# Performance work log

Measured on AMD Instinct MI355X. Metric: run time of the kernel, lower is better.

Reference implementation:

```python
import jax, jax.numpy as jnp
import numpy as np

ALPHA = 8.3  # depth-similarity decay from Depth-aware CNN
K = 3        # kernel size
PAD = 1      # padding (stride=1, dilation=1)


def _patches(x, k, pad):
    """Extract kxk stride-1 patches. x: (B,C,H,W) -> (B,C,k,k,H,W)."""
    B, C, H, W = x.shape
    xp = jnp.pad(x, ((0, 0), (0, 0), (pad, pad), (pad, pad)))
    rows = []
    for i in range(k):
        cols = [xp[:, :, i:i + H, j:j + W] for j in range(k)]
        rows.append(jnp.stack(cols, axis=2))          # (B,C,k,H,W)
    return jnp.stack(rows, axis=2)                     # (B,C,k,k,H,W)


def setup_inputs() -> dict:
    key = jax.random.key(0)
    k1, k2, k3 = jax.random.split(key, 3)
    B, Cin, H, W = 8, 512, 64, 64
    Cout = 64
    x = jax.random.normal(k1, (B, Cin, H, W), dtype=jnp.float32)
    depth = jax.random.uniform(k2, (B, 1, H, W), dtype=jnp.float32)
    stdv = 1.0 / np.sqrt(Cin * K * K)
    weight = jax.random.uniform(k3, (Cout, Cin, K, K), dtype=jnp.float32,
                                minval=-stdv, maxval=stdv)
    return {"input": x, "depth": depth, "weight": weight}


def reference(input, depth, weight):
    # depth-modulated conv: out(p0) = sum_pn w(pn) * x(p0+pn) * exp(-a*|d(p0)-d(p0+pn)|)
    xpat = _patches(input, K, PAD)                 # (B,Cin,K,K,H,W)
    dpat = _patches(depth, K, PAD)                 # (B,1,K,K,H,W)
    d0 = depth[:, :, None, None, :, :]             # center depth (B,1,1,1,H,W)
    gate = jnp.exp(-ALPHA * jnp.abs(d0 - dpat))    # (B,1,K,K,H,W)
    out = jnp.einsum('ocij,bcijhw->bohw', weight, xpat * gate)
    return out
```

## Files before the change

kernel.cpp:

```cpp
#include <hip/hip_runtime.h>
#include <math.h>

#define ALPHA 8.3f
#define XSZ   16896
#define WSZ   36864
#define BUFSZ 53760

typedef short v8s  __attribute__((ext_vector_type(8)));
typedef float v16f __attribute__((ext_vector_type(16)));
typedef float v4f  __attribute__((ext_vector_type(4)));

static __device__ __forceinline__ unsigned short f2bf(float f) {
    unsigned int u = __float_as_uint(f);
    u = (u + 0x7fffu + ((u >> 16) & 1u)) >> 16;
    return (unsigned short)u;
}

static __device__ __forceinline__ void async16(const void* g, void* l) {
    __builtin_amdgcn_global_load_lds(
        (const __attribute__((address_space(1))) unsigned int*)g,
        (__attribute__((address_space(3))) unsigned int*)l, 16, 0, 0);
}

__global__ __launch_bounds__(256) void prep_weights(const float* __restrict__ w,
                                                    unsigned short* __restrict__ wt) {
    const int i = blockIdx.x * 256 + threadIdx.x;
    if (i >= 294912) return;
    const int j    = i & 7;
    const int lane = (i >> 3) & 63;
    const int F    = i >> 9;
    const int kc   = F & 1;
    const int mt   = (F >> 1) & 1;
    const int tq   = F >> 2;
    const int tap  = tq % 9;
    const int ss   = tq / 9;
    const int o    = mt * 32 + (lane & 31);
    const int cin  = ss * 32 + kc * 16 + (lane >> 5) * 8 + j;
    wt[i] = f2bf(w[(o * 512 + cin) * 9 + tap]);
}

__global__ __launch_bounds__(384)
void depthconv_v15(const float* __restrict__ x,
                   const float* __restrict__ depth,
                   const unsigned short* __restrict__ wt,
                   float* __restrict__ out) {
    __shared__ __align__(16) char smem[2 * BUFSZ];

    const int bx   = blockIdx.x;
    const int xcd  = bx & 7;
    const int i0   = bx >> 3;
    const int b    = i0 & 7;
    const int h0   = (xcd * 4 + (i0 >> 3)) * 2;

    const int tid  = threadIdx.x;
    const int wid  = tid >> 6;
    const int lane = tid & 63;
    const int l31  = lane & 31;
    const int half = lane >> 5;
    const int rt   = wid & 1;
    const int di   = wid >> 1;

    const float* xb = x + (size_t)b * 2097152;
    const float* xsrc[3];
    int  goff[3];
    bool gval[3], gact[3];
#pragma unroll
    for (int it = 0; it < 3; ++it) {
        const int g_i = it * 384 + tid;
        const bool act = (g_i < 1056);
        const int p_ = g_i / 264;
        const int s_ = g_i - p_ * 264;
        const int r_ = s_ / 66, c_ = s_ - r_ * 66;
        const int hh = h0 - 1 + r_, ww = c_ - 1;
        const bool val = act && hh >= 0 && hh < 64 && ww >= 0 && ww < 64;
        gact[it] = act;
        gval[it] = val;
        goff[it] = g_i * 16;
        xsrc[it] = val ? (xb + (size_t)(p_ * 8) * 4096 + hh * 64 + ww) : xb;
    }

#define XLOAD(SS, V)                                                             \
    {                                                                            \
        const size_t adv = (size_t)(SS) * 131072;       \
        _Pragma("unroll")                                                        \
        for (int it = 0; it < 3; ++it)                                           \
            _Pragma("unroll")                                                    \
            for (int e = 0; e < 8; ++e)                                          \
                V[it][e] = gval[it] ? xsrc[it][adv + (size_t)e * 4096] : 0.f;    \
    }
#define XWRITE(V, BSEL)                                                          \
    {                                                                            \
        char* dx = smem + (BSEL) * BUFSZ;                                        \
        _Pragma("unroll")                                                        \
        for (int it = 0; it < 3; ++it)                                           \
            if (gact[it]) {                                                      \
                uint4 u;                                                         \
                u.x = f2bf(V[it][0]) | ((unsigned)f2bf(V[it][1]) << 16);         \
                u.y = f2bf(V[it][2]) | ((unsigned)f2bf(V[it][3]) << 16);         \
                u.z = f2bf(V[it][4]) | ((unsigned)f2bf(V[it][5]) << 16);         \
                u.w = f2bf(V[it][6]) | ((unsigned)f2bf(V[it][7]) << 16);         \
                *(uint4*)(dx + goff[it]) = u;                                    \
            }                                                                    \
    }
#define WISSUE(SS, BSEL)                                                         \
    {                                                                            \
        char* dw = smem + (BSEL) * BUFSZ + XSZ;                                  \
        const char* ws = (const char*)wt + (size_t)(SS) * WSZ;                   \
        _Pragma("unroll")                                                        \
        for (int k = 0; k < 6; ++k)                                              \
            async16(ws + (size_t)(k * 384 + tid) * 16,                           \
                    dw + (k * 384 + tid) * 16);                                  \
    }

    float gt[2][3];
    {
        const float* dp = depth + (size_t)b * 4096;
        const int hq = h0 + rt;
        const int hn = hq + di - 1;
#pragma unroll
        for (int n = 0; n < 2; ++n) {
            const int wq = n * 32 + l31;
            const float d0 = dp[hq * 64 + wq];
#pragma unroll
            for (int dj = 0; dj < 3; ++dj) {
                const int wn = wq + dj - 1;
                const float dn = (hn >= 0 && hn < 64 && wn >= 0 && wn < 64)
                                     ? dp[hn * 64 + wn] : 0.f;
                gt[n][dj] = __expf(-ALPHA * fabsf(d0 - dn));
            }
        }
    }

    v16f a00[3], a01[3], a10[3], a11[3];
#pragma unroll
    for (int d = 0; d < 3; ++d)
#pragma unroll
        for (int r = 0; r < 16; ++r) { a00[d][r] = 0.f; a01[d][r] = 0.f;
                                       a10[d][r] = 0.f; a11[d][r] = 0.f; }

    const int aOff = XSZ + di * 12288 + lane * 16;
    const int bOff = (half * 264 + (rt + di) * 66 + l31) * 16;

    float v[3][8];
    WISSUE(0, 0);
    XLOAD(0, v);
    XWRITE(v, 0);

    for (int ss = 0; ss < 16; ++ss) {
        __syncthreads();
        const int cur = ss & 1;
        const int nxt = cur ^ 1;
        if (ss < 15) {
            WISSUE(ss + 1, nxt);
            XLOAD(ss + 1, v);
        }
        const char* ba = smem + cur * BUFSZ + aOff;
        const char* bb = smem + cur * BUFSZ + bOff;
#pragma unroll
        for (int dj = 0; dj < 3; ++dj) {
#pragma unroll
            for (int kc = 0; kc < 2; ++kc) {
                const v8s w0 = *(const v8s*)(ba + ((dj * 2 + 0) * 2 + kc) * 1024);
                const v8s w1 = *(const v8s*)(ba + ((dj * 2 + 1) * 2 + kc) * 1024);
                const v8s x0 = *(const v8s*)(bb + kc * 8448 + (0 * 32 + dj) * 16);
                const v8s x1 = *(const v8s*)(bb + kc * 8448 + (1 * 32 + dj) * 16);
                a00[dj] = __builtin_amdgcn_mfma_f32_32x32x16_bf16(w0, x0, a00[dj], 0, 0, 0);
                a01[dj] = __builtin_amdgcn_mfma_f32_32x32x16_bf16(w1, x0, a01[dj], 0, 0, 0);
                a10[dj] = __builtin_amdgcn_mfma_f32_32x32x16_bf16(w0, x1, a10[dj], 0, 0, 0);
                a11[dj] = __builtin_amdgcn_mfma_f32_32x32x16_bf16(w1, x1, a11[dj], 0, 0, 0);
            }
        }
        if (ss < 15) XWRITE(v, nxt);
    }

#pragma unroll
    for (int r = 0; r < 16; ++r) {
        a00[0][r] = gt[0][0] * a00[0][r];
        a00[0][r] = fmaf(gt[0][1], a00[1][r], a00[0][r]);
        a00[0][r] = fmaf(gt[0][2], a00[2][r], a00[0][r]);
        a01[0][r] = gt[0][0] * a01[0][r];
        a01[0][r] = fmaf(gt[0][1], a01[1][r], a01[0][r]);
        a01[0][r] = fmaf(gt[0][2], a01[2][r], a01[0][r]);
        a10[0][r] = gt[1][0] * a10[0][r];
        a10[0][r] = fmaf(gt[1][1], a10[1][r], a10[0][r]);
        a10[0][r] = fmaf(gt[1][2], a10[2][r], a10[0][r]);
        a11[0][r] = gt[1][0] * a11[0][r];
        a11[0][r] = fmaf(gt[1][1], a11[1][r], a11[0][r]);
        a11[0][r] = fmaf(gt[1][2], a11[2][r], a11[0][r]);
    }

    __syncthreads();
    float* red = (float*)smem;
    const int rbase = rt * 4096 + lane * 4;
#define EPI_STORE(ACC, N, MT)                                                    \
    _Pragma("unroll")                                                            \
    for (int qd = 0; qd < 4; ++qd) {                                             \
        v4f vv; vv[0] = ACC[0][qd * 4]; vv[1] = ACC[0][qd * 4 + 1];              \
        vv[2] = ACC[0][qd * 4 + 2]; vv[3] = ACC[0][qd * 4 + 3];                  \
        *(v4f*)&red[rbase + ((N) * 2 + (MT)) * 1024 + qd * 256] = vv;            \
    }
#define EPI_ADD(ACC, N, MT)                                                      \
    _Pragma("unroll")                                                            \
    for (int qd = 0; qd < 4; ++qd) {                                             \
        v4f vv = *(const v4f*)&red[rbase + ((N) * 2 + (MT)) * 1024 + qd * 256];  \
        vv[0] += ACC[0][qd * 4];     vv[1] += ACC[0][qd * 4 + 1];                \
        vv[2] += ACC[0][qd * 4 + 2]; vv[3] += ACC[0][qd * 4 + 3];                \
        *(v4f*)&red[rbase + ((N) * 2 + (MT)) * 1024 + qd * 256] = vv;            \
    }
    if (di == 2) {
        EPI_STORE(a00, 0, 0) EPI_STORE(a01, 0, 1) EPI_STORE(a10, 1, 0) EPI_STORE(a11, 1, 1)
    }
    __syncthreads();
    if (di == 1) {
        EPI_ADD(a00, 0, 0) EPI_ADD(a01, 0, 1) EPI_ADD(a10, 1, 0) EPI_ADD(a11, 1, 1)
    }
    __syncthreads();
    if (di == 0) {
        float* ob = out + (size_t)b * 262144 + (h0 + rt) * 64;
#define EPI_OUT(ACC, N, MT)                                                      \
    _Pragma("unroll")                                                            \
    for (int qd = 0; qd < 4; ++qd) {                                             \
        const v4f vv = *(const v4f*)&red[rbase + ((N) * 2 + (MT)) * 1024 + qd * 256]; \
        _Pragma("unroll")                                                        \
        for (int j = 0; j < 4; ++j) {                                            \
            const int rg = qd * 4 + j;                                           \
            const int o = (MT) * 32 + (rg & 3) + 8 * (rg >> 2) + 4 * half;       \
            ob[(size_t)o * 4096 + (N) * 32 + l31] = ACC[0][rg] + vv[j];          \
        }                                                                        \
    }
        EPI_OUT(a00, 0, 0) EPI_OUT(a01, 0, 1) EPI_OUT(a10, 1, 0) EPI_OUT(a11, 1, 1)
    }
}

extern "C" void kernel_launch(void* const* d_in, const int* in_sizes, int n_in,
                              void* d_out, int out_size, void* d_ws, size_t ws_size,
                              hipStream_t stream) {
    const float* x      = (const float*)d_in[0];
    const float* depth  = (const float*)d_in[1];
    const float* weight = (const float*)d_in[2];
    float* out = (float*)d_out;

    unsigned short* wtb = (unsigned short*)d_ws;

    prep_weights<<<1152, 256, 0, stream>>>(weight, wtb);
    depthconv_v15<<<256, 384, 0, stream>>>(x, depth, wtb, out);
}
```

Before: 133.0 us.

## Split output channels across twice the waves and software-pipeline loads with manual waitcnt

Doubles the block to 768 threads so each wave owns one 32-channel output tile instead of two, halving its accumulator registers. The staging loop becomes a two-register-set software pipeline: the next slice's global loads are issued before the current compute, and raw s_waitcnt plus s_barrier replace __syncthreads. Depth-gate computation moves after the main loop to shorten live ranges. This aims to hide memory latency and raise per-CU wave count, at the cost of fragile hand-counted vmcnt values and more LDS reads of the shared x tiles.

```diff
diff --git a/kernel.cpp b/kernel.cpp
--- a/kernel.cpp
+++ b/kernel.cpp
@@ -39,8 +39,8 @@
     wt[i] = f2bf(w[(o * 512 + cin) * 9 + tap]);
 }
 
-__global__ __launch_bounds__(384)
-void depthconv_v15(const float* __restrict__ x,
+__global__ __launch_bounds__(768, 3)
+void depthconv_v16(const float* __restrict__ x,
                    const float* __restrict__ depth,
                    const unsigned short* __restrict__ wt,
                    float* __restrict__ out) {
@@ -57,60 +57,132 @@
     const int lane = tid & 63;
     const int l31  = lane & 31;
     const int half = lane >> 5;
-    const int rt   = wid & 1;
-    const int di   = wid >> 1;
+    const int mt   = wid & 1;
+    const int rt   = (wid >> 1) & 1;
+    const int di   = wid >> 2;
 
     const float* xb = x + (size_t)b * 2097152;
-    const float* xsrc[3];
-    int  goff[3];
-    bool gval[3], gact[3];
-#pragma unroll
-    for (int it = 0; it < 3; ++it) {
-        const int g_i = it * 384 + tid;
-        const bool act = (g_i < 1056);
-        const int p_ = g_i / 264;
-        const int s_ = g_i - p_ * 264;
-        const int r_ = s_ / 66, c_ = s_ - r_ * 66;
-        const int hh = h0 - 1 + r_, ww = c_ - 1;
-        const bool val = act && hh >= 0 && hh < 64 && ww >= 0 && ww < 64;
-        gact[it] = act;
-        gval[it] = val;
-        goff[it] = g_i * 16;
-        xsrc[it] = val ? (xb + (size_t)(p_ * 8) * 4096 + hh * 64 + ww) : xb;
-    }
-
-#define XLOAD(SS, V)                                                             \
-    {                                                                            \
-        const size_t adv = (size_t)(SS) * 131072;       \
-        _Pragma("unroll")                                                        \
-        for (int it = 0; it < 3; ++it)                                           \
+
+    int goff0, goff1; bool val0, val1, act1;
+    const float* pX0; const float* pX1;
+    {
+        const int g0 = tid;
+        const int p0 = g0 / 264, s0 = g0 - p0 * 264;
+        const int r0 = s0 / 66,  c0 = s0 - r0 * 66;
+        const int hh0 = h0 - 1 + r0, ww0 = c0 - 1;
+        val0  = (hh0 >= 0 && hh0 < 64 && ww0 >= 0 && ww0 < 64);
+        goff0 = g0 * 16;
+        pX0   = val0 ? (xb + (size_t)(p0 * 8) * 4096 + hh0 * 64 + ww0) : xb;
+
+        act1 = (tid < 288);
+        const int g1 = act1 ? (768 + tid) : tid;
+        const int p1 = g1 / 264, s1 = g1 - p1 * 264;
+        const int r1 = s1 / 66,  c1 = s1 - r1 * 66;
+        const int hh1 = h0 - 1 + r1, ww1 = c1 - 1;
+        val1  = (hh1 >= 0 && hh1 < 64 && ww1 >= 0 && ww1 < 64);
+        goff1 = g1 * 16;
+        pX1   = val1 ? (xb + (size_t)(p1 * 8) * 4096 + hh1 * 64 + ww1) : xb;
+    }
+    const char* pW = (const char*)wt;
+
+#define XLOAD(V)                                                                 \
+    {                                                                            \
+        _Pragma("unroll")                                                        \
+        for (int e = 0; e < 8; ++e) V[e]     = pX0[(size_t)e * 4096];            \
+        _Pragma("unroll")                                                        \
+        for (int e = 0; e < 8; ++e) V[8 + e] = pX1[(size_t)e * 4096];            \
+        pX0 += 131072; pX1 += 131072;                                            \
+    }
+#define XWRITE(V, BSEL)                                                          \
+    {                                                                            \
+        char* dx = smem + (BSEL) * BUFSZ;                                        \
+        uint4 u0;                                                                \
+        u0.x = f2bf(V[0]) | ((unsigned)f2bf(V[1]) << 16);                        \
+        u0.y = f2bf(V[2]) | ((unsigned)f2bf(V[3]) << 16);                        \
+        u0.z = f2bf(V[4]) | ((unsigned)f2bf(V[5]) << 16);                        \
+        u0.w = f2bf(V[6]) | ((unsigned)f2bf(V[7]) << 16);                        \
+        if (!val0) { u0.x = 0u; u0.y = 0u; u0.z = 0u; u0.w = 0u; }               \
+        *(uint4*)(dx + goff0) = u0;                                              \
+        if (act1) {                                                              \
+            uint4 u1;                                                            \
+            u1.x = f2bf(V[8])  | ((unsigned)f2bf(V[9])  << 16);                  \
+            u1.y = f2bf(V[10]) | ((unsigned)f2bf(V[11]) << 16);                  \
+            u1.z = f2bf(V[12]) | ((unsigned)f2bf(V[13]) << 16);                  \
+            u1.w = f2bf(V[14]) | ((unsigned)f2bf(V[15]) << 16);                  \
+            if (!val1) { u1.x = 0u; u1.y = 0u; u1.z = 0u; u1.w = 0u; }           \
+            *(uint4*)(dx + goff1) = u1;                                          \
+        }                                                                        \
+    }
+#define WISSUE(BSEL)                                                             \
+    {                                                                            \
+        char* dw = smem + (BSEL) * BUFSZ + XSZ;                                  \
+        _Pragma("unroll")                                                        \
+        for (int k = 0; k < 3; ++k)                                              \
+            async16(pW + (size_t)(k * 768 + tid) * 16,                           \
+                    dw + (k * 768 + tid) * 16);                                  \
+        pW += WSZ;                                                               \
+    }
+
+    v16f A0[3], A1[3];
+#pragma unroll
+    for (int d = 0; d < 3; ++d)
+#pragma unroll
+        for (int r = 0; r < 16; ++r) { A0[d][r] = 0.f; A1[d][r] = 0.f; }
+
+    const int aOff = XSZ + di * 12288 + mt * 2048 + lane * 16;
+    const int bOff = (half * 264 + (rt + di) * 66 + l31) * 16;
+
+#define COMPUTE(BSEL)                                                            \
+    {                                                                            \
+        const char* ba = smem + (BSEL) * BUFSZ + aOff;                           \
+        const char* bb = smem + (BSEL) * BUFSZ + bOff;                           \
+        _Pragma("unroll")                                                        \
+        for (int dj = 0; dj < 3; ++dj)                                           \
             _Pragma("unroll")                                                    \
-            for (int e = 0; e < 8; ++e)                                          \
-                V[it][e] = gval[it] ? xsrc[it][adv + (size_t)e * 4096] : 0.f;    \
-    }
-#define XWRITE(V, BSEL)                                                          \
-    {                                                                            \
-        char* dx = smem + (BSEL) * BUFSZ;                                        \
-        _Pragma("unroll")                                                        \
-        for (int it = 0; it < 3; ++it)                                           \
-            if (gact[it]) {                                                      \
-                uint4 u;                                                         \
-                u.x = f2bf(V[it][0]) | ((unsigned)f2bf(V[it][1]) << 16);         \
-                u.y = f2bf(V[it][2]) | ((unsigned)f2bf(V[it][3]) << 16);         \
-                u.z = f2bf(V[it][4]) | ((unsigned)f2bf(V[it][5]) << 16);         \
-                u.w = f2bf(V[it][6]) | ((unsigned)f2bf(V[it][7]) << 16);         \
-                *(uint4*)(dx + goff[it]) = u;                                    \
+            for (int kc = 0; kc < 2; ++kc) {                                     \
+                const v8s wv = *(const v8s*)(ba + dj * 4096 + kc * 1024);        \
+                const v8s x0 = *(const v8s*)(bb + kc * 8448 + dj * 16);          \
+                const v8s x1 = *(const v8s*)(bb + kc * 8448 + 512 + dj * 16);    \
+                A0[dj] = __builtin_amdgcn_mfma_f32_32x32x16_bf16(wv, x0, A0[dj], 0, 0, 0); \
+                A1[dj] = __builtin_amdgcn_mfma_f32_32x32x16_bf16(wv, x1, A1[dj], 0, 0, 0); \
             }                                                                    \
     }
-#define WISSUE(SS, BSEL)                                                         \
-    {                                                                            \
-        char* dw = smem + (BSEL) * BUFSZ + XSZ;                                  \
-        const char* ws = (const char*)wt + (size_t)(SS) * WSZ;                   \
-        _Pragma("unroll")                                                        \
-        for (int k = 0; k < 6; ++k)                                              \
-            async16(ws + (size_t)(k * 384 + tid) * 16,                           \
-                    dw + (k * 384 + tid) * 16);                                  \
-    }
+
+    float vA[16], vB[16];
+
+    XLOAD(vA);
+    WISSUE(0);
+    XLOAD(vB);
+    asm volatile("s_waitcnt vmcnt(19)" ::: "memory");
+    XWRITE(vA, 0);
+    asm volatile("s_waitcnt vmcnt(16) lgkmcnt(0)" ::: "memory");
+    __builtin_amdgcn_s_barrier();
+    __builtin_amdgcn_sched_barrier(0);
+
+#define PHASE_STD(CUR, VNEXT, VFREE)                                             \
+    {                                                                            \
+        WISSUE(CUR ^ 1);                                     \
+        XLOAD(VFREE);                                               \
+        COMPUTE(CUR);                                                            \
+        asm volatile("s_waitcnt vmcnt(19)" ::: "memory");    \
+        XWRITE(VNEXT, CUR ^ 1);                                                  \
+        asm volatile("s_waitcnt vmcnt(16) lgkmcnt(0)" ::: "memory");             \
+        __builtin_amdgcn_s_barrier();                                            \
+        __builtin_amdgcn_sched_barrier(0);                                       \
+    }
+
+    for (int sp = 0; sp < 7; ++sp) {
+        PHASE_STD(0, vB, vA);
+        PHASE_STD(1, vA, vB);
+    }
+    WISSUE(1);
+    COMPUTE(0);
+    asm volatile("s_waitcnt vmcnt(3)" ::: "memory");
+    XWRITE(vB, 1);
+    asm volatile("s_waitcnt vmcnt(0) lgkmcnt(0)" ::: "memory");
+    __builtin_amdgcn_s_barrier();
+    __builtin_amdgcn_sched_barrier(0);
+    COMPUTE(1);
 
     float gt[2][3];
     {
@@ -131,104 +203,52 @@
         }
     }
 
-    v16f a00[3], a01[3], a10[3], a11[3];
-#pragma unroll
-    for (int d = 0; d < 3; ++d)
-#pragma unroll
-        for (int r = 0; r < 16; ++r) { a00[d][r] = 0.f; a01[d][r] = 0.f;
-                                       a10[d][r] = 0.f; a11[d][r] = 0.f; }
-
-    const int aOff = XSZ + di * 12288 + lane * 16;
-    const int bOff = (half * 264 + (rt + di) * 66 + l31) * 16;
-
-    float v[3][8];
-    WISSUE(0, 0);
-    XLOAD(0, v);
-    XWRITE(v, 0);
-
-    for (int ss = 0; ss < 16; ++ss) {
-        __syncthreads();
-        const int cur = ss & 1;
-        const int nxt = cur ^ 1;
-        if (ss < 15) {
-            WISSUE(ss + 1, nxt);
-            XLOAD(ss + 1, v);
-        }
-        const char* ba = smem + cur * BUFSZ + aOff;
-        const char* bb = smem + cur * BUFSZ + bOff;
-#pragma unroll
-        for (int dj = 0; dj < 3; ++dj) {
-#pragma unroll
-            for (int kc = 0; kc < 2; ++kc) {
-                const v8s w0 = *(const v8s*)(ba + ((dj * 2 + 0) * 2 + kc) * 1024);
-                const v8s w1 = *(const v8s*)(ba + ((dj * 2 + 1) * 2 + kc) * 1024);
-                const v8s x0 = *(const v8s*)(bb + kc * 8448 + (0 * 32 + dj) * 16);
-                const v8s x1 = *(const v8s*)(bb + kc * 8448 + (1 * 32 + dj) * 16);
-                a00[dj] = __builtin_amdgcn_mfma_f32_32x32x16_bf16(w0, x0, a00[dj], 0, 0, 0);
-                a01[dj] = __builtin_amdgcn_mfma_f32_32x32x16_bf16(w1, x0, a01[dj], 0, 0, 0);
-                a10[dj] = __builtin_amdgcn_mfma_f32_32x32x16_bf16(w0, x1, a10[dj], 0, 0, 0);
-                a11[dj] = __builtin_amdgcn_mfma_f32_32x32x16_bf16(w1, x1, a11[dj], 0, 0, 0);
-            }
-        }
-        if (ss < 15) XWRITE(v, nxt);
-    }
-
 #pragma unroll
     for (int r = 0; r < 16; ++r) {
-        a00[0][r] = gt[0][0] * a00[0][r];
-        a00[0][r] = fmaf(gt[0][1], a00[1][r], a00[0][r]);
-        a00[0][r] = fmaf(gt[0][2], a00[2][r], a00[0][r]);
-        a01[0][r] = gt[0][0] * a01[0][r];
-        a01[0][r] = fmaf(gt[0][1], a01[1][r], a01[0][r]);
-        a01[0][r] = fmaf(gt[0][2], a01[2][r], a01[0][r]);
-        a10[0][r] = gt[1][0] * a10[0][r];
-        a10[0][r] = fmaf(gt[1][1], a10[1][r], a10[0][r]);
-        a10[0][r] = fmaf(gt[1][2], a10[2][r], a10[0][r]);
-        a11[0][r] = gt[1][0] * a11[0][r];
-        a11[0][r] = fmaf(gt[1][1], a11[1][r], a11[0][r]);
-        a11[0][r] = fmaf(gt[1][2], a11[2][r], a11[0][r]);
+        A0[0][r] = gt[0][0] * A0[0][r];
+        A0[0][r] = fmaf(gt[0][1], A0[1][r], A0[0][r]);
+        A0[0][r] = fmaf(gt[0][2], A0[2][r], A0[0][r]);
+        A1[0][r] = gt[1][0] * A1[0][r];
+        A1[0][r] = fmaf(gt[1][1], A1[1][r], A1[0][r]);
+        A1[0][r] = fmaf(gt[1][2], A1[2][r], A1[0][r]);
     }
 
     __syncthreads();
     float* red = (float*)smem;
     const int rbase = rt * 4096 + lane * 4;
-#define EPI_STORE(ACC, N, MT)                                                    \
+#define EPI_STORE(ACC, N)                                                        \
     _Pragma("unroll")                                                            \
     for (int qd = 0; qd < 4; ++qd) {                                             \
         v4f vv; vv[0] = ACC[0][qd * 4]; vv[1] = ACC[0][qd * 4 + 1];              \
         vv[2] = ACC[0][qd * 4 + 2]; vv[3] = ACC[0][qd * 4 + 3];                  \
-        *(v4f*)&red[rbase + ((N) * 2 + (MT)) * 1024 + qd * 256] = vv;            \
-    }
-#define EPI_ADD(ACC, N, MT)                                                      \
+        *(v4f*)&red[rbase + ((N) * 2 + mt) * 1024 + qd * 256] = vv;              \
+    }
+#define EPI_ADD(ACC, N)                                                          \
     _Pragma("unroll")                                                            \
     for (int qd = 0; qd < 4; ++qd) {                                             \
-        v4f vv = *(const v4f*)&red[rbase + ((N) * 2 + (MT)) * 1024 + qd * 256];  \
+        v4f vv = *(const v4f*)&red[rbase + ((N) * 2 + mt) * 1024 + qd * 256];    \
         vv[0] += ACC[0][qd * 4];     vv[1] += ACC[0][qd * 4 + 1];                \
         vv[2] += ACC[0][qd * 4 + 2]; vv[3] += ACC[0][qd * 4 + 3];                \
-        *(v4f*)&red[rbase + ((N) * 2 + (MT)) * 1024 + qd * 256] = vv;            \
-    }
-    if (di == 2) {
-        EPI_STORE(a00, 0, 0) EPI_STORE(a01, 0, 1) EPI_STORE(a10, 1, 0) EPI_STORE(a11, 1, 1)
-    }
+        *(v4f*)&red[rbase + ((N) * 2 + mt) * 1024 + qd * 256] = vv;              \
+    }
+    if (di == 2) { EPI_STORE(A0, 0) EPI_STORE(A1, 1) }
     __syncthreads();
-    if (di == 1) {
-        EPI_ADD(a00, 0, 0) EPI_ADD(a01, 0, 1) EPI_ADD(a10, 1, 0) EPI_ADD(a11, 1, 1)
-    }
+    if (di == 1) { EPI_ADD(A0, 0) EPI_ADD(A1, 1) }
     __syncthreads();
     if (di == 0) {
         float* ob = out + (size_t)b * 262144 + (h0 + rt) * 64;
-#define EPI_OUT(ACC, N, MT)                                                      \
+#define EPI_OUT(ACC, N)                                                          \
     _Pragma("unroll")                                                            \
     for (int qd = 0; qd < 4; ++qd) {                                             \
-        const v4f vv = *(const v4f*)&red[rbase + ((N) * 2 + (MT)) * 1024 + qd * 256]; \
+        const v4f vv = *(const v4f*)&red[rbase + ((N) * 2 + mt) * 1024 + qd * 256]; \
         _Pragma("unroll")                                                        \
         for (int j = 0; j < 4; ++j) {                                            \
             const int rg = qd * 4 + j;                                           \
-            const int o = (MT) * 32 + (rg & 3) + 8 * (rg >> 2) + 4 * half;       \
+            const int o = mt * 32 + (rg & 3) + 8 * (rg >> 2) + 4 * half;         \
             ob[(size_t)o * 4096 + (N) * 32 + l31] = ACC[0][rg] + vv[j];          \
         }                                                                        \
     }
-        EPI_OUT(a00, 0, 0) EPI_OUT(a01, 0, 1) EPI_OUT(a10, 1, 0) EPI_OUT(a11, 1, 1)
+        EPI_OUT(A0, 0) EPI_OUT(A1, 1)
     }
 }
 
@@ -243,5 +263,5 @@
     unsigned short* wtb = (unsigned short*)d_ws;
 
     prep_weights<<<1152, 256, 0, stream>>>(weight, wtb);
-    depthconv_v15<<<256, 384, 0, stream>>>(x, depth, wtb, out);
-}
+    depthconv_v16<<<256, 768, 0, stream>>>(x, depth, wtb, out);
+}
```

New measurement: 122.1 us. -8.2%, faster.
